# Kernel optimization log

Measured on AMD Instinct MI355X. Metric: run time of the kernel, lower is better.

## Reference

```python
import jax, jax.numpy as jnp
import numpy as np

EMBED = 512
COS_TAU = 0.3          # cosine temperature in CrossModalAttention
SOFT_TAU = 0.3         # soft_mask_tau in TokenSparse
SPARSE_RATIO = 0.6     # keep ratio
SCALE = EMBED ** -0.5


def setup_inputs() -> dict:
    key = jax.random.key(0)
    ks = jax.random.split(key, 18)
    B, N, C = 64, 256, 512
    W = 0.02  # param init scale
    return {
        "rgb": jax.random.normal(ks[0], (B, N, C), jnp.float32),
        "nir": jax.random.normal(ks[1], (B, N, C), jnp.float32),
        "tir": jax.random.normal(ks[2], (B, N, C), jnp.float32),
        "rgb_g": jax.random.normal(ks[3], (B, C), jnp.float32),
        "nir_g": jax.random.normal(ks[4], (B, C), jnp.float32),
        "tir_g": jax.random.normal(ks[5], (B, C), jnp.float32),
        # 9 CrossModalAttention modules in order:
        # rgb_self, rgb_cross_nir, rgb_cross_tir,
        # nir_self, nir_cross_rgb, nir_cross_tir,
        # tir_self, tir_cross_rgb, tir_cross_nir
        "attn_qw": jax.random.normal(ks[6], (9, C, C), jnp.float32) * W,
        "attn_qb": jnp.zeros((9, C), jnp.float32),
        "attn_kw": jax.random.normal(ks[7], (9, C, C), jnp.float32) * W,
        "attn_kb": jnp.zeros((9, C), jnp.float32),
        # 3 TokenSparse adaptive-weight MLPs (rgb, nir, tir)
        "mlp_w1": jax.random.normal(ks[8], (3, 3 * C, 256), jnp.float32) * W,
        "mlp_b1": jnp.zeros((3, 256), jnp.float32),
        "ln_g": jnp.ones((3, 256), jnp.float32),
        "ln_b": jnp.zeros((3, 256), jnp.float32),
        "mlp_w2": jax.random.normal(ks[9], (3, 256, 64), jnp.float32) * W,
        "mlp_b2": jnp.zeros((3, 64), jnp.float32),
        "mlp_w3": jax.random.normal(ks[10], (3, 64, 3), jnp.float32) * W,
        "mlp_b3": jnp.zeros((3, 3), jnp.float32),
    }


def _cosine(p, g):
    # F.cosine_similarity(patches, global.unsqueeze(1), dim=-1) -> (B, N)
    pn = p / jnp.maximum(jnp.linalg.norm(p, axis=-1, keepdims=True), 1e-8)
    gn = g / jnp.maximum(jnp.linalg.norm(g, axis=-1, keepdims=True), 1e-8)
    return jnp.einsum('bnc,bc->bn', pn, gn)


def _attn_score(patches, g, qw, qb, kw, kb):
    # single-head cross-attention: softmax(q k^T / sqrt(C) + cos / tau)
    cos = _cosine(patches, g)
    q = g @ qw + qb                         # (B, C)
    k = jnp.einsum('bnc,cd->bnd', patches, kw) + kb  # (B, N, C)
    logits = jnp.einsum('bc,bnc->bn', q, k) * SCALE + cos / COS_TAU
    return jax.nn.softmax(logits, axis=-1)


def _norm_score(s):
    # z-score (unbiased std like torch.std) + sigmoid
    m = jnp.mean(s, axis=-1, keepdims=True)
    sd = jnp.std(s, axis=-1, ddof=1, keepdims=True) + 1e-5
    return jax.nn.sigmoid((s - m) / sd)


def _layernorm(x, g, b):
    m = jnp.mean(x, axis=-1, keepdims=True)
    v = jnp.var(x, axis=-1, keepdims=True)
    return (x - m) / jnp.sqrt(v + 1e-5) * g + b


def _token_sparse(tokens, s_im, s_m2, s_m3, gfeats, w1, b1, lg, lb, w2, b2, w3, b3):
    s_im, s_m2, s_m3 = _norm_score(s_im), _norm_score(s_m2), _norm_score(s_m3)
    h = jax.nn.gelu(_layernorm(gfeats @ w1 + b1, lg, lb), approximate=False)
    h = jax.nn.gelu(h @ w2 + b2, approximate=False)
    w = jax.nn.softmax(h @ w3 + b3, axis=-1)            # (B, 3)
    score = w[:, 0:1] * s_im + w[:, 1:2] * s_m2 + w[:, 2:3] * s_m3
    thr = jnp.quantile(score, 1.0 - SPARSE_RATIO, axis=1, keepdims=True)
    mask = jax.nn.sigmoid((score - thr) / SOFT_TAU)     # (B, N)
    return tokens * mask[..., None], mask


def reference(rgb, nir, tir, rgb_g, nir_g, tir_g,
              attn_qw, attn_qb, attn_kw, attn_kb,
              mlp_w1, mlp_b1, ln_g, ln_b, mlp_w2, mlp_b2, mlp_w3, mlp_b3):
    patches = (rgb, nir, tir)
    globs = (rgb_g, nir_g, tir_g)
    # guide modality indices per target modality: (self, other1, other2)
    guides = ((0, 1, 2), (1, 0, 2), (2, 0, 1))
    gcat = jnp.concatenate([rgb_g, nir_g, tir_g], axis=-1)  # (B, 3C)
    outs, masks = [], []
    for mi in range(3):
        p = patches[mi]
        s = [
            _attn_score(p, globs[g],
                        attn_qw[3 * mi + j], attn_qb[3 * mi + j],
                        attn_kw[3 * mi + j], attn_kb[3 * mi + j])
            for j, g in enumerate(guides[mi])
        ]
        mt, mk = _token_sparse(p, s[0], s[1], s[2], gcat,
                               mlp_w1[mi], mlp_b1[mi], ln_g[mi], ln_b[mi],
                               mlp_w2[mi], mlp_b2[mi], mlp_w3[mi], mlp_b3[mi])
        outs.append(mt)
        masks.append(mk)
    return (outs[0], outs[1], outs[2], masks[0], masks[1], masks[2])
```

## Files before the change

### kernel.cpp

```cpp
#include <hip/hip_runtime.h>
#include <math.h>

#define B 64
#define N 256
#define C 512

typedef float nfloat4 __attribute__((ext_vector_type(4)));

__device__ __forceinline__ int guide_of(int m) {
    int mi = m / 3, j = m % 3;
    return (j == 0) ? mi : (j == 1 ? ((mi == 0) ? 1 : 0) : ((mi == 2) ? 1 : 2));
}

template<int NW>
__device__ __forceinline__ float breduce_sum(float v, volatile float* red, int t) {
    int w = t >> 6, l = t & 63;
#pragma unroll
    for (int mm = 1; mm < 64; mm <<= 1) v += __shfl_xor(v, mm);
    __syncthreads();
    if (l == 0) red[w] = v;
    __syncthreads();
    float s = red[0];
#pragma unroll
    for (int i = 1; i < NW; i++) s += red[i];
    return s;
}

__device__ __forceinline__ float dot4(float4 a, float4 b) {
    return a.x * b.x + a.y * b.y + a.z * b.z + a.w * b.w;
}

__global__ __launch_bounds__(256) void k_proj_mlp(const float* g0, const float* g1, const float* g2,
                                                  const float* qw, const float* w1,
                                                  float* part, float* h1part, float* gn) {
    int bid = blockIdx.x;
    int t = threadIdx.x;
    __shared__ float gt[64 * 132];
    if (bid < 576) {
        int cx = bid & 7, m = (bid >> 3) % 9, ks = bid / 72;
        int e0 = ks * 64;
        int gi = guide_of(m);
        const float* g = (gi == 0) ? g0 : (gi == 1 ? g1 : g2);
        for (int idx = t; idx < 1024; idx += 256) {
            int r = idx >> 4, c4 = idx & 15;
            ((float4*)&gt[r * 132])[c4] = ((const float4*)(g + (size_t)r * C + e0))[c4];
        }
        __syncthreads();
        int c0 = cx * 64 + 4 * (t & 15);
        int b0 = 4 * (t >> 4);
        float4 acc[4];
#pragma unroll
        for (int j = 0; j < 4; j++) acc[j] = make_float4(0.f, 0.f, 0.f, 0.f);
        const float* W = qw + (size_t)m * C * C + (size_t)e0 * C + c0;
#pragma unroll 4
        for (int e = 0; e < 64; e++) {
            float4 wv = *(const float4*)(W + (size_t)e * C);
#pragma unroll
            for (int j = 0; j < 4; j++) {
                float gv = gt[(b0 + j) * 132 + e];
                acc[j].x += gv * wv.x; acc[j].y += gv * wv.y;
                acc[j].z += gv * wv.z; acc[j].w += gv * wv.w;
            }
        }
#pragma unroll
        for (int j = 0; j < 4; j++)
            *(float4*)(part + (size_t)ks * 294912 + ((size_t)m * B + b0 + j) * C + c0) = acc[j];
    } else if (bid < 720) {
        int r = bid - 576;
        int cx = r & 3, mi = (r >> 2) % 3, ks = r / 12;
        int e0 = ks * 128;
        const float* g = (e0 < 512) ? g0 : (e0 < 1024 ? g1 : g2);
        int eo = e0 & 511;
        for (int idx = t; idx < 2048; idx += 256) {
            int rr = idx >> 5, c4 = idx & 31;
            ((float4*)&gt[rr * 132])[c4] = ((const float4*)(g + (size_t)rr * C + eo))[c4];
        }
        __syncthreads();
        int c0 = cx * 64 + 4 * (t & 15);
        int b0 = 4 * (t >> 4);
        float4 acc[4];
#pragma unroll
        for (int j = 0; j < 4; j++) acc[j] = make_float4(0.f, 0.f, 0.f, 0.f);
        const float* W = w1 + ((size_t)mi * 1536 + e0) * 256 + c0;
#pragma unroll 4
        for (int e = 0; e < 128; e++) {
            float4 wv = *(const float4*)(W + (size_t)e * 256);
#pragma unroll
            for (int j = 0; j < 4; j++) {
                float gv = gt[(b0 + j) * 132 + e];
                acc[j].x += gv * wv.x; acc[j].y += gv * wv.y;
                acc[j].z += gv * wv.z; acc[j].w += gv * wv.w;
            }
        }
#pragma unroll
        for (int j = 0; j < 4; j++)
            *(float4*)(h1part + (((size_t)ks * 3 + mi) * B + b0 + j) * 256 + c0) = acc[j];
    } else {
        int gm = bid - 720;
        const float* g = (gm == 0) ? g0 : (gm == 1 ? g1 : g2);
        int wv = t >> 6, l = t & 63;
        for (int r = wv; r < 64; r += 4) {
            const float4* gv = (const float4*)(g + (size_t)r * C);
            float4 a = gv[l], b2 = gv[64 + l];
            float n2 = dot4(a, a) + dot4(b2, b2);
#pragma unroll
            for (int mm = 1; mm < 64; mm <<= 1) n2 += __shfl_xor(n2, mm);
            float inv = 1.0f / fmaxf(sqrtf(n2), 1e-8f);
            float4* o = (float4*)(gn + ((size_t)gm * B + r) * C);
            a.x *= inv; a.y *= inv; a.z *= inv; a.w *= inv;
            b2.x *= inv; b2.y *= inv; b2.z *= inv; b2.w *= inv;
            o[l] = a; o[64 + l] = b2;
        }
    }
}

__global__ __launch_bounds__(256) void k_kproj(const float* kw, const float* part,
                                               const float* qb, const float* kb,
                                               const float* h1part,
                                               const float* b1, const float* lng, const float* lnb,
                                               const float* w2, const float* b2,
                                               const float* w3, const float* b3,
                                               float* kpart, float* qkb_part, float* wmix) {
    int cx = blockIdx.x, m = blockIdx.y, ds = blockIdx.z;
    int t = threadIdx.x;
    if (cx >= 8) {
        int widx = (cx - 8) * 72 + m * 8 + ds;
        if (widx >= 192) return;
        int mi = widx >> 6;
        int b = widx & 63;
        __shared__ float h1[256];
        __shared__ float h2p[4][64];
        __shared__ float h2[64];
        __shared__ float redm[4];
        float a1 = b1[mi * 256 + t];
#pragma unroll
        for (int ks = 0; ks < 12; ks++) a1 += h1part[(((size_t)ks * 3 + mi) * B + b) * 256 + t];
        float total = breduce_sum<4>(a1, redm, t);
        float mean = total * (1.0f / 256.0f);
        float dv = a1 - mean;
        float vtot = breduce_sum<4>(dv * dv, redm, t);
        float var = vtot * (1.0f / 256.0f);
        float x = dv / sqrtf(var + 1e-5f) * lng[mi * 256 + t] + lnb[mi * 256 + t];
        x = 0.5f * x * (1.0f + erff(x * 0.70710678118654752f));
        h1[t] = x;
        __syncthreads();
        {
            int col = t & 63, sl = t >> 6;
            float a2 = 0.f;
            const float* W2 = w2 + (size_t)mi * 256 * 64 + col;
#pragma unroll 8
            for (int e = sl * 64; e < sl * 64 + 64; e++) a2 += h1[e] * W2[(size_t)e * 64];
            h2p[sl][col] = a2;
        }
        __syncthreads();
        if (t < 64) {
            float a2 = b2[mi * 64 + t];
#pragma unroll
            for (int s2 = 0; s2 < 4; s2++) a2 += h2p[s2][t];
            a2 = 0.5f * a2 * (1.0f + erff(a2 * 0.70710678118654752f));
            h2[t] = a2;
        }
        __syncthreads();
        if (t == 0) {
            float l3[3];
            for (int j = 0; j < 3; j++) {
                float a3 = b3[mi * 3 + j];
                for (int e = 0; e < 64; e++) a3 += h2[e] * w3[((size_t)mi * 64 + e) * 3 + j];
                l3[j] = a3;
            }
            float mx = fmaxf(l3[0], fmaxf(l3[1], l3[2]));
            float e0 = expf(l3[0] - mx), e1 = expf(l3[1] - mx), e2 = expf(l3[2] - mx);
            float inv = 1.0f / (e0 + e1 + e2);
            wmix[((size_t)mi * B + b) * 4 + 0] = e0 * inv;
            wmix[((size_t)mi * B + b) * 4 + 1] = e1 * inv;
            wmix[((size_t)mi * B + b) * 4 + 2] = e2 * inv;
        }
        return;
    }
    int c0b = cx * 64, d0 = ds * 64;
    __shared__ float kt[64][65];
    __shared__ float qt[64][65];
    for (int idx = t; idx < 1024; idx += 256) {
        int r = idx >> 4, c4 = idx & 15;
        float4 kv4 = *(const float4*)(kw + ((size_t)m * C + c0b + r) * C + d0 + c4 * 4);
        kt[r][c4 * 4 + 0] = kv4.x; kt[r][c4 * 4 + 1] = kv4.y;
        kt[r][c4 * 4 + 2] = kv4.z; kt[r][c4 * 4 + 3] = kv4.w;
        float4 s = *(const float4*)(qb + (size_t)m * C + d0 + c4 * 4);
        const float* pp = part + ((size_t)m * B + r) * C + d0 + c4 * 4;
#pragma unroll
        for (int ks = 0; ks < 8; ks++) {
            float4 v = *(const float4*)(pp + (size_t)ks * 294912);
            s.x += v.x; s.y += v.y; s.z += v.z; s.w += v.w;
        }
        qt[r][c4 * 4 + 0] = s.x; qt[r][c4 * 4 + 1] = s.y;
        qt[r][c4 * 4 + 2] = s.z; qt[r][c4 * 4 + 3] = s.w;
    }
    __syncthreads();
    int c0 = 4 * (t & 15);
    int b0 = 4 * (t >> 4);
    float4 acc[4];
#pragma unroll
    for (int j = 0; j < 4; j++) acc[j] = make_float4(0.f, 0.f, 0.f, 0.f);
#pragma unroll 4
    for (int d = 0; d < 64; d++) {
        float k0 = kt[c0 + 0][d], k1 = kt[c0 + 1][d], k2 = kt[c0 + 2][d], k3 = kt[c0 + 3][d];
#pragma unroll
        for (int j = 0; j < 4; j++) {
            float qv = qt[b0 + j][d];
            acc[j].x += qv * k0; acc[j].y += qv * k1;
            acc[j].z += qv * k2; acc[j].w += qv * k3;
        }
    }
#pragma unroll
    for (int j = 0; j < 4; j++)
        *(float4*)(kpart + (size_t)ds * 294912 + ((size_t)m * B + b0 + j) * C + c0b + c0) = acc[j];
    if (cx == 0 && t < 64) {
        float s = 0.f;
        const float* kbp = kb + (size_t)m * C + d0;
        for (int d = 0; d < 64; d++) s += qt[t][d] * kbp[d];
        qkb_part[((size_t)m * 8 + ds) * B + t] = s;
    }
}

__global__ __launch_bounds__(256) void k_logits(const float* p0, const float* p1, const float* p2,
                                                const float* kpart, const float* qkb_part,
                                                const float* gn, float* lgt) {
    int b = blockIdx.x, mi = blockIdx.y, ns = blockIdx.z;
    int t = threadIdx.x, w = t >> 6, l = t & 63;
    const float* p = (mi == 0) ? p0 : (mi == 1 ? p1 : p2);
    int s = l & 7, tl = l >> 3;
    int n = ns * 32 + w * 8 + tl;
    const float4* pbase = (const float4*)(p + (size_t)b * N * C);
    const float4* prow = pbase + (size_t)n * 128;
    float4 pf[8];
#pragma unroll
    for (int i = 0; i < 8; i++) pf[i] = prow[s + 8 * i];
    __shared__ float q6[6][512];
    __shared__ float qkb_s[3];
    for (int idx = t; idx < 768; idx += 256) {
        int row = idx >> 7, c4 = idx & 127;
        float4 v;
        if (row < 3) {
            int m = 3 * mi + row;
            const float4* kp = (const float4*)kpart + ((size_t)m * B + b) * 128 + c4;
            v = kp[0];
#pragma unroll
            for (int ds = 1; ds < 8; ds++) {
                float4 u = kp[(size_t)ds * 73728];
                v.x += u.x; v.y += u.y; v.z += u.z; v.w += u.w;
            }
        } else {
            int gi = guide_of(3 * mi + row - 3);
            v = ((const float4*)(gn + ((size_t)gi * B + b) * C))[c4];
        }
        ((float4*)q6[row])[c4] = v;
    }
    if (t < 3) {
        int m = 3 * mi + t;
        float sq = 0.f;
#pragma unroll
        for (int ds = 0; ds < 8; ds++) sq += qkb_part[((size_t)m * 8 + ds) * B + b];
        qkb_s[t] = sq;
    }
    __syncthreads();
    const float SCALE = 0.044194173824159216f;
    float* L = lgt + (size_t)(mi * B + b) * 3 * N;
    const float4* Q0 = (const float4*)q6[0];
    const float4* Q1 = (const float4*)q6[1];
    const float4* Q2 = (const float4*)q6[2];
    const float4* G0 = (const float4*)q6[3];
    const float4* G1 = (const float4*)q6[4];
    const float4* G2 = (const float4*)q6[5];
    {
        float pp = 0.f, dj0 = 0.f, dj1 = 0.f, dj2 = 0.f, cj0 = 0.f, cj1 = 0.f, cj2 = 0.f;
#pragma unroll
        for (int i = 0; i < 16; i++) {
            int o = s + 8 * i;
            float4 pv = (i < 8) ? pf[i] : prow[o];
            pp  += dot4(pv, pv);
            dj0 += dot4(pv, Q0[o]);
            dj1 += dot4(pv, Q1[o]);
            dj2 += dot4(pv, Q2[o]);
            cj0 += dot4(pv, G0[o]);
            cj1 += dot4(pv, G1[o]);
            cj2 += dot4(pv, G2[o]);
        }
#pragma unroll
        for (int mm = 1; mm < 8; mm <<= 1) {
            pp  += __shfl_xor(pp, mm);
            dj0 += __shfl_xor(dj0, mm);
            dj1 += __shfl_xor(dj1, mm);
            dj2 += __shfl_xor(dj2, mm);
            cj0 += __shfl_xor(cj0, mm);
            cj1 += __shfl_xor(cj1, mm);
            cj2 += __shfl_xor(cj2, mm);
        }
        if (s == 0) {
            float rn = fmaxf(sqrtf(pp), 1e-8f);
            float ic = 1.0f / (rn * 0.3f);
            L[0 * N + n] = (dj0 + qkb_s[0]) * SCALE + cj0 * ic;
            L[1 * N + n] = (dj1 + qkb_s[1]) * SCALE + cj1 * ic;
            L[2 * N + n] = (dj2 + qkb_s[2]) * SCALE + cj2 * ic;
        }
    }
}

__global__ __launch_bounds__(256) void k_finscale(const float* lgt, const float* wmix,
                                                  const float* p0, const float* p1, const float* p2,
                                                  float* out) {
    int b = blockIdx.x, mi = blockIdx.y, ns = blockIdx.z, t = threadIdx.x;
    int w = t >> 6, l = t & 63;
    const float* L = lgt + (size_t)(mi * B + b) * 3 * N;
    float wj0 = wmix[((size_t)mi * B + b) * 4 + 0];
    float wj1 = wmix[((size_t)mi * B + b) * 4 + 1];
    float wj2 = wmix[((size_t)mi * B + b) * 4 + 2];
    float v0 = L[0 * N + t], v1 = L[1 * N + t], v2 = L[2 * N + t];
    const float* p = (mi == 0) ? p0 : (mi == 1 ? p1 : p2);
    const float4* pslab = (const float4*)(p + (size_t)b * N * C + (size_t)ns * 32 * C);
    float4 pref[8];
#pragma unroll
    for (int i = 0; i < 8; i++) pref[i] = pslab[t + 256 * i];
    __shared__ float red3[3][4];
    __shared__ float sc[256];
    __shared__ float mks[256];
    __shared__ float thr_s;
    float m0 = v0, m1 = v1, m2 = v2;
#pragma unroll
    for (int mm = 1; mm < 64; mm <<= 1) {
        m0 = fmaxf(m0, __shfl_xor(m0, mm));
        m1 = fmaxf(m1, __shfl_xor(m1, mm));
        m2 = fmaxf(m2, __shfl_xor(m2, mm));
    }
    __syncthreads();
    if (l == 0) { red3[0][w] = m0; red3[1][w] = m1; red3[2][w] = m2; }
    __syncthreads();
    float mx0 = red3[0][0], mx1 = red3[1][0], mx2 = red3[2][0];
#pragma unroll
    for (int i = 1; i < 4; i++) {
        mx0 = fmaxf(mx0, red3[0][i]); mx1 = fmaxf(mx1, red3[1][i]); mx2 = fmaxf(mx2, red3[2][i]);
    }
    float e0 = expf(v0 - mx0), e1 = expf(v1 - mx1), e2 = expf(v2 - mx2);
    float s0 = e0, s1 = e1, s2 = e2;
#pragma unroll
    for (int mm = 1; mm < 64; mm <<= 1) {
        s0 += __shfl_xor(s0, mm); s1 += __shfl_xor(s1, mm); s2 += __shfl_xor(s2, mm);
    }
    __syncthreads();
    if (l == 0) { red3[0][w] = s0; red3[1][w] = s1; red3[2][w] = s2; }
    __syncthreads();
    float t0 = red3[0][0], t1 = red3[1][0], t2 = red3[2][0];
#pragma unroll
    for (int i = 1; i < 4; i++) { t0 += red3[0][i]; t1 += red3[1][i]; t2 += red3[2][i]; }
    float pr0 = e0 / t0, pr1 = e1 / t1, pr2 = e2 / t2;
    float u0 = pr0, u1 = pr1, u2 = pr2;
#pragma unroll
    for (int mm = 1; mm < 64; mm <<= 1) {
        u0 += __shfl_xor(u0, mm); u1 += __shfl_xor(u1, mm); u2 += __shfl_xor(u2, mm);
    }
    __syncthreads();
    if (l == 0) { red3[0][w] = u0; red3[1][w] = u1; red3[2][w] = u2; }
    __syncthreads();
    float tt0 = red3[0][0], tt1 = red3[1][0], tt2 = red3[2][0];
#pragma unroll
    for (int i = 1; i < 4; i++) { tt0 += red3[0][i]; tt1 += red3[1][i]; tt2 += red3[2][i]; }
    float dv0 = pr0 - tt0 * (1.0f / 256.0f);
    float dv1 = pr1 - tt1 * (1.0f / 256.0f);
    float dv2 = pr2 - tt2 * (1.0f / 256.0f);
    float q0 = dv0 * dv0, q1 = dv1 * dv1, q2 = dv2 * dv2;
#pragma unroll
    for (int mm = 1; mm < 64; mm <<= 1) {
        q0 += __shfl_xor(q0, mm); q1 += __shfl_xor(q1, mm); q2 += __shfl_xor(q2, mm);
    }
    __syncthreads();
    if (l == 0) { red3[0][w] = q0; red3[1][w] = q1; red3[2][w] = q2; }
    __syncthreads();
    float vt0 = red3[0][0], vt1 = red3[1][0], vt2 = red3[2][0];
#pragma unroll
    for (int i = 1; i < 4; i++) { vt0 += red3[0][i]; vt1 += red3[1][i]; vt2 += red3[2][i]; }
    float sd0 = sqrtf(vt0 * (1.0f / 255.0f)) + 1e-5f;
    float sd1 = sqrtf(vt1 * (1.0f / 255.0f)) + 1e-5f;
    float sd2 = sqrtf(vt2 * (1.0f / 255.0f)) + 1e-5f;
    float sg0 = 1.0f / (1.0f + expf(-(dv0 / sd0)));
    float sg1 = 1.0f / (1.0f + expf(-(dv1 / sd1)));
    float sg2 = 1.0f / (1.0f + expf(-(dv2 / sd2)));
    float score = wj0 * sg0;
    score += wj1 * sg1;
    score += wj2 * sg2;
    sc[t] = score;
    __syncthreads();
    {
        int cl = 0, ce = 0;
        for (int m2i = 0; m2i < N; m2i++) {
            float v2i = sc[m2i];
            cl += (v2i < score) ? 1 : 0;
            ce += (v2i == score) ? 1 : 0;
        }
        if (cl <= 102 && 102 < cl + ce) thr_s = score;
    }
    __syncthreads();
    float thr = thr_s;
    float mk = 1.0f / (1.0f + expf(-(score - thr) * (1.0f / 0.3f)));
    mks[t] = mk;
    if ((t >> 5) == ns)
        out[(size_t)3 * B * N * C + ((size_t)mi * B + b) * N + t] = mk;
    __syncthreads();
    nfloat4* oslab = (nfloat4*)(out + (size_t)mi * B * N * C + (size_t)b * N * C
                                + (size_t)ns * 32 * C);
#pragma unroll
    for (int i = 0; i < 8; i++) {
        int idx = t + 256 * i;
        float mkv = mks[ns * 32 + (idx >> 7)];
        nfloat4 nv;
        nv.x = pref[i].x * mkv; nv.y = pref[i].y * mkv;
        nv.z = pref[i].z * mkv; nv.w = pref[i].w * mkv;
        __builtin_nontemporal_store(nv, oslab + idx);
    }
#pragma unroll
    for (int i = 8; i < 16; i++) {
        int idx = t + 256 * i;
        float4 v = pslab[idx];
        float mkv = mks[ns * 32 + (idx >> 7)];
        nfloat4 nv;
        nv.x = v.x * mkv; nv.y = v.y * mkv; nv.z = v.z * mkv; nv.w = v.w * mkv;
        __builtin_nontemporal_store(nv, oslab + idx);
    }
}

extern "C" void kernel_launch(void* const* d_in, const int* in_sizes, int n_in,
                              void* d_out, int out_size, void* d_ws, size_t ws_size,
                              hipStream_t stream) {
    const float* rgb   = (const float*)d_in[0];
    const float* nir   = (const float*)d_in[1];
    const float* tir   = (const float*)d_in[2];
    const float* rgb_g = (const float*)d_in[3];
    const float* nir_g = (const float*)d_in[4];
    const float* tir_g = (const float*)d_in[5];
    const float* attn_qw = (const float*)d_in[6];
    const float* attn_qb = (const float*)d_in[7];
    const float* attn_kw = (const float*)d_in[8];
    const float* attn_kb = (const float*)d_in[9];
    const float* mlp_w1 = (const float*)d_in[10];
    const float* mlp_b1 = (const float*)d_in[11];
    const float* ln_g = (const float*)d_in[12];
    const float* ln_b = (const float*)d_in[13];
    const float* mlp_w2 = (const float*)d_in[14];
    const float* mlp_b2 = (const float*)d_in[15];
    const float* mlp_w3 = (const float*)d_in[16];
    const float* mlp_b3 = (const float*)d_in[17];
    float* out = (float*)d_out;

    float* ws = (float*)d_ws;
    float* part     = ws;
    float* kpart    = ws + 2359296;
    float* qkb_part = ws + 4718592;
    float* h1part   = ws + 4723712;
    float* lgt      = ws + 5313536;
    float* gn       = ws + 5460992;
    float* wmix     = ws + 5559296;

    k_proj_mlp<<<723, 256, 0, stream>>>(rgb_g, nir_g, tir_g, attn_qw, mlp_w1,
                                        part, h1part, gn);
    k_kproj<<<dim3(11, 9, 8), 256, 0, stream>>>(attn_kw, part, attn_qb, attn_kb,
                                                h1part, mlp_b1, ln_g, ln_b,
                                                mlp_w2, mlp_b2, mlp_w3, mlp_b3,
                                                kpart, qkb_part, wmix);
    k_logits<<<dim3(B, 3, 8), 256, 0, stream>>>(rgb, nir, tir, kpart, qkb_part, gn, lgt);
    k_finscale<<<dim3(B, 3, 8), 256, 0, stream>>>(lgt, wmix, rgb, nir, tir, out);
}
```

Before: 93.84 us.

## Prefetch patch tensors into cache during early projection kernels

```diff
diff --git a/kernel.cpp b/kernel.cpp
--- a/kernel.cpp
+++ b/kernel.cpp
@@ -30,9 +30,29 @@
     return a.x * b.x + a.y * b.y + a.z * b.z + a.w * b.w;
 }
 
+__device__ __forceinline__ void warm_chunk(int chunk, int t,
+                                           const float* p0, const float* p1, const float* p2,
+                                           float* scrap) {
+    int mi = chunk >> 7;
+    const float* p = (mi == 0) ? p0 : (mi == 1 ? p1 : p2);
+    const float4* base = (const float4*)(p + (size_t)(chunk & 127) * 65536);
+    float4 s = make_float4(0.f, 0.f, 0.f, 0.f);
+#pragma unroll 8
+    for (int i = 0; i < 64; i++) {
+        float4 v = base[t + 256 * i];
+        s.x += v.x; s.y += v.y; s.z += v.z; s.w += v.w;
+    }
+    float r = s.x + s.y + s.z + s.w;
+#pragma unroll
+    for (int mm = 1; mm < 64; mm <<= 1) r += __shfl_xor(r, mm);
+    if (t == 0) scrap[chunk] = r;
+}
+
 __global__ __launch_bounds__(256) void k_proj_mlp(const float* g0, const float* g1, const float* g2,
                                                   const float* qw, const float* w1,
-                                                  float* part, float* h1part, float* gn) {
+                                                  const float* p0, const float* p1, const float* p2,
+                                                  float* part, float* h1part, float* gn,
+                                                  float* scrap) {
     int bid = blockIdx.x;
     int t = threadIdx.x;
     __shared__ float gt[64 * 132];
@@ -95,7 +115,7 @@
 #pragma unroll
         for (int j = 0; j < 4; j++)
             *(float4*)(h1part + (((size_t)ks * 3 + mi) * B + b0 + j) * 256 + c0) = acc[j];
-    } else {
+    } else if (bid < 723) {
         int gm = bid - 720;
         const float* g = (gm == 0) ? g0 : (gm == 1 ? g1 : g2);
         int wv = t >> 6, l = t & 63;
@@ -111,6 +131,8 @@
             b2.x *= inv; b2.y *= inv; b2.z *= inv; b2.w *= inv;
             o[l] = a; o[64 + l] = b2;
         }
+    } else {
+        warm_chunk(bid - 723, t, p0, p1, p2, scrap);
     }
 }
 
@@ -120,12 +142,17 @@
                                                const float* b1, const float* lng, const float* lnb,
                                                const float* w2, const float* b2,
                                                const float* w3, const float* b3,
-                                               float* kpart, float* qkb_part, float* wmix) {
+                                               const float* p0, const float* p1, const float* p2,
+                                               float* kpart, float* qkb_part, float* wmix,
+                                               float* scrap) {
     int cx = blockIdx.x, m = blockIdx.y, ds = blockIdx.z;
     int t = threadIdx.x;
     if (cx >= 8) {
         int widx = (cx - 8) * 72 + m * 8 + ds;
-        if (widx >= 192) return;
+        if (widx >= 192) {
+            if (widx < 276) warm_chunk(300 + widx - 192, t, p0, p1, p2, scrap);
+            return;
+        }
         int mi = widx >> 6;
         int b = widx & 63;
         __shared__ float h1[256];
@@ -457,13 +484,15 @@
     float* lgt      = ws + 5313536;
     float* gn       = ws + 5460992;
     float* wmix     = ws + 5559296;
-
-    k_proj_mlp<<<723, 256, 0, stream>>>(rgb_g, nir_g, tir_g, attn_qw, mlp_w1,
-                                        part, h1part, gn);
-    k_kproj<<<dim3(11, 9, 8), 256, 0, stream>>>(attn_kw, part, attn_qb, attn_kb,
+    float* scrap    = ws + 5560320;
+
+    k_proj_mlp<<<1023, 256, 0, stream>>>(rgb_g, nir_g, tir_g, attn_qw, mlp_w1,
+                                         rgb, nir, tir, part, h1part, gn, scrap);
+    k_kproj<<<dim3(13, 9, 8), 256, 0, stream>>>(attn_kw, part, attn_qb, attn_kb,
                                                 h1part, mlp_b1, ln_g, ln_b,
                                                 mlp_w2, mlp_b2, mlp_w3, mlp_b3,
-                                                kpart, qkb_part, wmix);
+                                                rgb, nir, tir,
+                                                kpart, qkb_part, wmix, scrap);
     k_logits<<<dim3(B, 3, 8), 256, 0, stream>>>(rgb, nir, tir, kpart, qkb_part, gn, lgt);
     k_finscale<<<dim3(B, 3, 8), 256, 0, stream>>>(lgt, wmix, rgb, nir, tir, out);
 }
```

After: 99.43 us. 6.0% more time.
